# Performance work log

Measured on AMD Instinct MI355X. Metric: run time of the kernel, lower is better.

## Reference

```python
import jax, jax.numpy as jnp
import numpy as np

def setup_inputs() -> dict:
    key = jax.random.key(0)
    k1, k2 = jax.random.split(key)
    B, D = 256, 512
    mu = jax.random.normal(k1, (B, D), dtype=jnp.float32)
    logvar = jax.random.normal(k2, (B, D), dtype=jnp.float32)
    return {"mu": mu, "logvar": logvar}

def reference(mu, logvar):
    # Pairwise KL( N(mu_i, var_i) || N(mu_j, var_j) ) for all i != j.
    B = mu.shape[0]
    var = jnp.exp(logvar)
    mu_i = mu[:, None, :]          # [B,1,D]
    mu_j = mu[None, :, :]          # [1,B,D]
    lv_i = logvar[:, None, :]
    lv_j = logvar[None, :, :]
    var_i = var[:, None, :]
    var_j = var[None, :, :]
    # kl[i,j] = 0.5 * sum_d (lv_j - lv_i + var_i/var_j + (mu_i-mu_j)^2/var_j - 1)
    kl = 0.5 * jnp.sum(lv_j - lv_i + var_i / var_j + (mu_i - mu_j) ** 2 / var_j - 1.0, axis=-1)  # [B,B]
    # exclude diagonal (i == j); note original divides by batch_size, not count
    mask = 1.0 - jnp.eye(B, dtype=kl.dtype)
    total = jnp.sum(kl * mask)
    return total / B
```

## Files before the change

kernel.cpp:

```cpp
#include <hip/hip_runtime.h>
#include <hip/hip_bf16.h>

#define BB 256
#define DD 512
#define NCHUNK 8
#define ROWS_PER_CHUNK (BB / NCHUNK)

__global__ void udl_phase1(const float* __restrict__ mu,
                           const float* __restrict__ lv,
                           float* __restrict__ ws) {
    const int d = threadIdx.x;
    const int chunk = blockIdx.x;
    const int row0 = chunk * ROWS_PER_CHUNK;

    float A = 0.f, P = 0.f, M = 0.f, Q = 0.f, R = 0.f;
#pragma unroll 4
    for (int r = 0; r < ROWS_PER_CHUNK; ++r) {
        const int idx = (row0 + r) * DD + d;
        const float m = mu[idx];
        const float l = lv[idx];
        const float ev = __expf(l);
        const float iv = __expf(-l);
        A += ev + m * m;
        P += iv;
        M += m;
        const float miv = m * iv;
        Q += miv;
        R += m * miv;
    }
    float* o = ws + (size_t)chunk * 5 * DD;
    o[0 * DD + d] = A;
    o[1 * DD + d] = P;
    o[2 * DD + d] = M;
    o[3 * DD + d] = Q;
    o[4 * DD + d] = R;
}

__global__ void udl_phase2(const float* __restrict__ ws,
                           float* __restrict__ out) {
    const int d = threadIdx.x;
    float A = 0.f, P = 0.f, M = 0.f, Q = 0.f, R = 0.f;
#pragma unroll
    for (int c = 0; c < NCHUNK; ++c) {
        const float* o = ws + (size_t)c * 5 * DD;
        A += o[0 * DD + d];
        P += o[1 * DD + d];
        M += o[2 * DD + d];
        Q += o[3 * DD + d];
        R += o[4 * DD + d];
    }
    double cd = (double)A * (double)P
              - 2.0 * (double)M * (double)Q
              + (double)BB * (double)R;

    for (int off = 32; off > 0; off >>= 1)
        cd += __shfl_down(cd, off, 64);

    __shared__ double sred[DD / 64];
    const int wid = threadIdx.x >> 6;
    const int lane = threadIdx.x & 63;
    if (lane == 0) sred[wid] = cd;
    __syncthreads();

    if (threadIdx.x == 0) {
        double full = 0.0;
#pragma unroll
        for (int w = 0; w < DD / 64; ++w) full += sred[w];
        const double result = (full - (double)DD * (double)BB * (double)BB)
                              / (2.0 * (double)BB);
        out[0] = (float)result;
    }
}

extern "C" void kernel_launch(void* const* d_in, const int* in_sizes, int n_in,
                              void* d_out, int out_size, void* d_ws, size_t ws_size,
                              hipStream_t stream) {
    const float* mu = (const float*)d_in[0];
    const float* lv = (const float*)d_in[1];
    float* out = (float*)d_out;
    float* ws = (float*)d_ws;

    udl_phase1<<<NCHUNK, DD, 0, stream>>>(mu, lv, ws);
    udl_phase2<<<1, DD, 0, stream>>>(ws, out);
}
```

Measured before the change: 60.40 us.

## Fuse two-phase reduction into a single 1024-thread block kernel

Replaces the 8-block partial-sum kernel plus a separate finalize kernel with one kernel launched as a single 1024-thread block. Two halves of the block each accumulate over 128 rows, combine through shared memory, and reduce to the scalar in place. This removes the second launch and the workspace round trip. In exchange, all memory traffic now runs on a single CU with longer serial loops per thread.

```diff
diff --git a/kernel.cpp b/kernel.cpp
--- a/kernel.cpp
+++ b/kernel.cpp
@@ -3,19 +3,17 @@
 
 #define BB 256
 #define DD 512
-#define NCHUNK 8
-#define ROWS_PER_CHUNK (BB / NCHUNK)
 
-__global__ void udl_phase1(const float* __restrict__ mu,
-                           const float* __restrict__ lv,
-                           float* __restrict__ ws) {
-    const int d = threadIdx.x;
-    const int chunk = blockIdx.x;
-    const int row0 = chunk * ROWS_PER_CHUNK;
+__global__ __launch_bounds__(1024) void udl_fused(const float* __restrict__ mu,
+                                                  const float* __restrict__ lv,
+                                                  float* __restrict__ out) {
+    const int d = threadIdx.x & (DD - 1);
+    const int h = threadIdx.x >> 9;
+    const int row0 = h * (BB / 2);
 
     float A = 0.f, P = 0.f, M = 0.f, Q = 0.f, R = 0.f;
-#pragma unroll 4
-    for (int r = 0; r < ROWS_PER_CHUNK; ++r) {
+#pragma unroll 8
+    for (int r = 0; r < BB / 2; ++r) {
         const int idx = (row0 + r) * DD + d;
         const float m = mu[idx];
         const float l = lv[idx];
@@ -28,35 +26,25 @@
         Q += miv;
         R += m * miv;
     }
-    float* o = ws + (size_t)chunk * 5 * DD;
-    o[0 * DD + d] = A;
-    o[1 * DD + d] = P;
-    o[2 * DD + d] = M;
-    o[3 * DD + d] = Q;
-    o[4 * DD + d] = R;
-}
 
-__global__ void udl_phase2(const float* __restrict__ ws,
-                           float* __restrict__ out) {
-    const int d = threadIdx.x;
-    float A = 0.f, P = 0.f, M = 0.f, Q = 0.f, R = 0.f;
-#pragma unroll
-    for (int c = 0; c < NCHUNK; ++c) {
-        const float* o = ws + (size_t)c * 5 * DD;
-        A += o[0 * DD + d];
-        P += o[1 * DD + d];
-        M += o[2 * DD + d];
-        Q += o[3 * DD + d];
-        R += o[4 * DD + d];
+    __shared__ float sA[DD], sP[DD], sM[DD], sQ[DD], sR[DD];
+    if (h == 1) { sA[d] = A; sP[d] = P; sM[d] = M; sQ[d] = Q; sR[d] = R; }
+    __syncthreads();
+
+    double cd = 0.0;
+    if (h == 0) {
+        const double Af = (double)A + (double)sA[d];
+        const double Pf = (double)P + (double)sP[d];
+        const double Mf = (double)M + (double)sM[d];
+        const double Qf = (double)Q + (double)sQ[d];
+        const double Rf = (double)R + (double)sR[d];
+        cd = Af * Pf - 2.0 * Mf * Qf + (double)BB * Rf;
     }
-    double cd = (double)A * (double)P
-              - 2.0 * (double)M * (double)Q
-              + (double)BB * (double)R;
 
     for (int off = 32; off > 0; off >>= 1)
         cd += __shfl_down(cd, off, 64);
 
-    __shared__ double sred[DD / 64];
+    __shared__ double sred[1024 / 64];
     const int wid = threadIdx.x >> 6;
     const int lane = threadIdx.x & 63;
     if (lane == 0) sred[wid] = cd;
@@ -65,7 +53,7 @@
     if (threadIdx.x == 0) {
         double full = 0.0;
 #pragma unroll
-        for (int w = 0; w < DD / 64; ++w) full += sred[w];
+        for (int w = 0; w < 1024 / 64; ++w) full += sred[w];
         const double result = (full - (double)DD * (double)BB * (double)BB)
                               / (2.0 * (double)BB);
         out[0] = (float)result;
@@ -78,8 +66,6 @@
     const float* mu = (const float*)d_in[0];
     const float* lv = (const float*)d_in[1];
     float* out = (float*)d_out;
-    float* ws = (float*)d_ws;
 
-    udl_phase1<<<NCHUNK, DD, 0, stream>>>(mu, lv, ws);
-    udl_phase2<<<1, DD, 0, stream>>>(ws, out);
+    udl_fused<<<1, 1024, 0, stream>>>(mu, lv, out);
 }
```

Measured after the change: 69.84 us. +15.6%, slower.
